# Performance work log

Hardware: AMD Instinct MI355X
Metric: run time of the kernel (lower is better)

The kernel has to match this reference:

```python
import jax, jax.numpy as jnp
import numpy as np

# ---- config (mirrors init_kwargs) ----
H = 128
W = 128
FMO_STEPS = 4
INPUT_FRAMES = 1
N_PIECES = 1
N_TERMS = 2
CAM_DIST = 2.0
ROT_DIVIDE = 1.0
SIGMAINV = 7000.0
ERODE_K = 5
FOCAL = float(1.0 / np.tan(1.57 / 4.0))  # generate_perspective_projection(1.57/2), aspect=1


def quaternion_to_angle_axis(q):
    # q: [B,4] in (w,x,y,z) convention (torchgeometry)
    q1, q2, q3 = q[..., 1], q[..., 2], q[..., 3]
    sin_sq = q1 * q1 + q2 * q2 + q3 * q3
    sin_t = jnp.sqrt(sin_sq + 1e-20)
    cos_t = q[..., 0]
    two_theta = 2.0 * jnp.where(cos_t < 0.0, jnp.arctan2(-sin_t, -cos_t), jnp.arctan2(sin_t, cos_t))
    k = jnp.where(sin_sq > 1e-12, two_theta / sin_t, 2.0)
    return q[..., 1:4] * k[..., None]


def angle_axis_to_rotation_matrix(aa):
    # aa: [B,3] -> [B,3,3] (Rodrigues)
    th = jnp.sqrt(jnp.sum(aa * aa, axis=-1, keepdims=True) + 1e-12)  # [B,1]
    k = aa / th
    kx, ky, kz = k[..., 0], k[..., 1], k[..., 2]
    zero = jnp.zeros_like(kx)
    K = jnp.stack([jnp.stack([zero, -kz, ky], -1),
                   jnp.stack([kz, zero, -kx], -1),
                   jnp.stack([-ky, kx, zero], -1)], -2)
    s = jnp.sin(th)[..., None]
    c = jnp.cos(th)[..., None]
    return jnp.eye(3, dtype=aa.dtype) + s * K + (1.0 - c) * jnp.matmul(K, K)


def rasterize(fv_img, fv_z, face_feat, fn_z):
    # fv_img [B,F,3,2] NDC, fv_z [B,F,3] camera z, face_feat [B,F,3,C], fn_z [B,F]
    B, F = fv_img.shape[:2]
    xs = jnp.linspace(-1.0, 1.0, W)
    ys = jnp.linspace(1.0, -1.0, H)
    py, px = jnp.meshgrid(ys, xs, indexing='ij')  # [H,W]
    a, b, c = fv_img[:, :, 0], fv_img[:, :, 1], fv_img[:, :, 2]  # [B,F,2]
    e0 = b - a
    e1 = c - a
    denom = e0[..., 0] * e1[..., 1] - e0[..., 1] * e1[..., 0]  # [B,F]
    valid = (fn_z > 0.0) & (jnp.abs(denom) > 1e-10)
    inv_den = jnp.where(jnp.abs(denom) > 1e-10, 1.0 / denom, 0.0)
    dx = px[None, None] - a[..., 0][..., None, None]  # [B,F,H,W]
    dy = py[None, None] - a[..., 1][..., None, None]
    w1 = (dx * e1[..., 1][..., None, None] - dy * e1[..., 0][..., None, None]) * inv_den[..., None, None]
    w2 = (e0[..., 0][..., None, None] * dy - e0[..., 1][..., None, None] * dx) * inv_den[..., None, None]
    w0 = 1.0 - w1 - w2
    inside = (w0 >= 0.0) & (w1 >= 0.0) & (w2 >= 0.0) & valid[..., None, None]
    zi = (w0 * fv_z[:, :, 0, None, None] + w1 * fv_z[:, :, 1, None, None] + w2 * fv_z[:, :, 2, None, None])
    score = jnp.where(inside, zi, -1e10)  # camera looks down -z: nearest face has max z
    best = jnp.argmax(score, axis=1)      # [B,H,W] z-buffer winner
    hit = jnp.any(inside, axis=1)
    bary = jnp.stack([w0, w1, w2], axis=-1)  # [B,F,H,W,3]
    idx = jnp.broadcast_to(best[:, None, :, :, None], (B, 1, H, W, 3))
    bary_b = jnp.take_along_axis(bary, idx, axis=1)[:, 0]  # [B,H,W,3]
    feat_b = jax.vmap(lambda f, i: f[i])(face_feat, best)  # [B,H,W,3,C]
    feats = jnp.einsum('bhwkc,bhwk->bhwc', feat_b, bary_b) * hit[..., None]
    # DIB-R soft silhouette: A = 1 - prod(1 - exp(-sigmainv*d^2)), d = dist to triangle, 0 inside
    d2 = None
    tri = (a, b, c)
    for i in range(3):
        p, q = tri[i], tri[(i + 1) % 3]
        ex = (q - p)[..., 0][..., None, None]
        ey = (q - p)[..., 1][..., None, None]
        rx = px[None, None] - p[..., 0][..., None, None]
        ry = py[None, None] - p[..., 1][..., None, None]
        L2 = ex * ex + ey * ey + 1e-12
        t = jnp.clip((rx * ex + ry * ey) / L2, 0.0, 1.0)
        dxe = rx - t * ex
        dye = ry - t * ey
        dd = dxe * dxe + dye * dye
        d2 = dd if d2 is None else jnp.minimum(d2, dd)
    d2 = jnp.where(inside, 0.0, d2)
    prob = jnp.where(valid[..., None, None], jnp.exp(-SIGMAINV * d2), 0.0)
    mask = 1.0 - jnp.prod(1.0 - prob, axis=1)  # [B,H,W]
    return feats, mask


def texture_sample(tex, uv):
    # tex [B,3,Th,Tw], uv [B,H,W,2] in [0,1]; bilinear, v axis flipped (image row 0 <-> v=1)
    Th, Tw = tex.shape[2], tex.shape[3]
    u = jnp.clip(uv[..., 0], 0.0, 1.0) * (Tw - 1)
    v = (1.0 - jnp.clip(uv[..., 1], 0.0, 1.0)) * (Th - 1)
    x0 = jnp.floor(u)
    y0 = jnp.floor(v)
    fx = (u - x0)[:, None]  # [B,1,H,W]
    fy = (v - y0)[:, None]
    x0i = jnp.clip(x0.astype(jnp.int32), 0, Tw - 1)
    x1i = jnp.clip(x0i + 1, 0, Tw - 1)
    y0i = jnp.clip(y0.astype(jnp.int32), 0, Th - 1)
    y1i = jnp.clip(y0i + 1, 0, Th - 1)
    g = jax.vmap(lambda t, yy, xx: t[:, yy, xx])  # [B,3,H,W]
    t00 = g(tex, y0i, x0i)
    t01 = g(tex, y0i, x1i)
    t10 = g(tex, y1i, x0i)
    t11 = g(tex, y1i, x1i)
    return t00 * (1 - fx) * (1 - fy) + t01 * fx * (1 - fy) + t10 * (1 - fx) * fy + t11 * fx * fy


def erode(m, k):
    # kornia erosion with an all-ones kxk kernel == min-pool (geodesic border)
    return -jax.lax.reduce_window(-m, -jnp.inf, jax.lax.max, (1, k, k), (1, 1, 1), 'SAME')


def render_frame(verts_world, faces, face_features, texture_maps):
    # camera at (0,0,CAM_DIST) looking at origin with up=(0,1,0): R_cam == I
    v_cam = verts_world - jnp.array([0.0, 0.0, CAM_DIST], dtype=verts_world.dtype)
    fv_cam = v_cam[:, faces]  # [B,F,3,3]
    n = jnp.cross(fv_cam[:, :, 1] - fv_cam[:, :, 0], fv_cam[:, :, 2] - fv_cam[:, :, 0])
    n = n / (jnp.linalg.norm(n, axis=-1, keepdims=True) + 1e-10)
    fn_z = n[..., 2]
    z = fv_cam[..., 2]  # negative in front of camera
    img = FOCAL * fv_cam[..., :2] / (-z[..., None] + 1e-10)  # [B,F,3,2]
    uv, mask = rasterize(img, z, face_features, fn_z)
    rgb = texture_sample(texture_maps, uv)  # [B,3,H,W]
    mask_e = erode(mask, ERODE_K)
    return jnp.concatenate([rgb, mask_e[:, None]], axis=1)  # [B,4,H,W]


def reference(vertices, translation, quaternion, exp, face_features, texture_maps, faces):
    rot = angle_axis_to_rotation_matrix(quaternion_to_angle_axis(quaternion[:, 0, 0]))
    trans_start = translation[:, :, 0, 0]  # [B,1,3]
    all_renders = []
    renders = []
    frames = 0
    time_before = 0.0
    for pind in range(N_PIECES):
        angles = quaternion_to_angle_axis(quaternion[:, pind, 1]) / ROT_DIVIDE
        rot_step = angle_axis_to_rotation_matrix(exp * angles / FMO_STEPS)
        rot_noexp = angle_axis_to_rotation_matrix(angles * (1.0 - exp))
        n_steps = FMO_STEPS * INPUT_FRAMES // N_PIECES  # prop[pind] (forced for single piece)
        for ti in np.linspace(0.0, 1.0, n_steps):
            if frames == 0:
                time_before = ti
            time_exp = time_before + (ti - time_before) * exp  # [1]
            verts = jnp.einsum('bij,bvj->bvi', rot, vertices) + trans_start
            for p in range(1, N_TERMS):
                verts = verts + (time_exp ** p) * translation[:, :, pind, p]
            renders.append(render_frame(verts, faces, face_features, texture_maps))
            frames += 1
            if frames == FMO_STEPS:
                frames = 0
                all_renders.append(jnp.stack(renders, 1))
                renders = []
                rot = jnp.matmul(rot, rot_noexp)
            else:
                rot = jnp.matmul(rot, rot_step)
        for p in range(1, N_TERMS):
            trans_start = trans_start + translation[:, :, pind, p]
    return jnp.stack(all_renders, 1)  # [B, input_frames, fmo_steps, 4, H, W]


def setup_inputs() -> dict:
    key = jax.random.key(0)
    ks = jax.random.split(key, 7)
    B, V, F = 1, 162, 320
    vertices = jax.random.normal(ks[0], (B, V, 3), jnp.float32) * 0.3
    translation = jax.random.normal(ks[1], (B, 1, N_PIECES, N_TERMS, 3), jnp.float32) * 0.1
    quaternion = jax.random.normal(ks[2], (B, N_PIECES, 2, 4), jnp.float32)
    exp = jax.random.uniform(ks[3], (1,), jnp.float32)
    face_features = jax.random.uniform(ks[4], (B, F, 3, 2), jnp.float32)
    texture_maps = jax.random.uniform(ks[5], (B, 3, 256, 256), jnp.float32)
    faces = jax.random.randint(ks[6], (F, 3), 0, V)
    return {"vertices": vertices, "translation": translation, "quaternion": quaternion,
            "exp": exp, "face_features": face_features, "texture_maps": texture_maps,
            "faces": faces}
```

## Files before the change

kernel.cpp:

```cpp
#include <hip/hip_runtime.h>
#include <math.h>

#define N_FRAMES 4
#define N_FACES  320
#define N_VERTS  162
#define IMG_H    128
#define IMG_W    128
#define FD_STRIDE 20
#define CHUNKS   8



__device__ __forceinline__ void q_to_aa(const float* q, float* aa) {
    float q1 = q[1], q2 = q[2], q3 = q[3];
    float sin_sq = (q1 * q1 + q2 * q2) + q3 * q3;
    float sin_t = sqrtf(sin_sq + 1e-20f);
    float cos_t = q[0];
    float two_theta = (cos_t < 0.0f) ? (2.0f * atan2f(-sin_t, -cos_t))
                                     : (2.0f * atan2f(sin_t, cos_t));
    float k = (sin_sq > 1e-12f) ? (two_theta / sin_t) : 2.0f;
    aa[0] = q1 * k; aa[1] = q2 * k; aa[2] = q3 * k;
}

__device__ __forceinline__ void aa_to_R(const float* aa, float* R) {
    float th = sqrtf(((aa[0] * aa[0] + aa[1] * aa[1]) + aa[2] * aa[2]) + 1e-12f);
    float kx = aa[0] / th, ky = aa[1] / th, kz = aa[2] / th;
    float K[9] = { 0.0f, -kz,  ky,
                   kz,  0.0f, -kx,
                  -ky,   kx, 0.0f };
    float s = sinf(th), c = cosf(th);
    float KK[9];
    for (int i = 0; i < 3; ++i)
        for (int j = 0; j < 3; ++j)
            KK[i*3+j] = (K[i*3+0] * K[0*3+j] + K[i*3+1] * K[1*3+j]) + K[i*3+2] * K[2*3+j];
    float omc = 1.0f - c;
    for (int i = 0; i < 9; ++i) {
        float eye = (i == 0 || i == 4 || i == 8) ? 1.0f : 0.0f;
        R[i] = (eye + s * K[i]) + omc * KK[i];
    }
}

__device__ __forceinline__ void mat3mul(const float* A, const float* B, float* C) {
    for (int i = 0; i < 3; ++i)
        for (int j = 0; j < 3; ++j)
            C[i*3+j] = (A[i*3+0] * B[0*3+j] + A[i*3+1] * B[1*3+j]) + A[i*3+2] * B[2*3+j];
}


__global__ void __launch_bounds__(256)
setup_kernel(const float* __restrict__ verts_in,
             const float* __restrict__ transl,
             const float* __restrict__ quat,
             const float* __restrict__ expv,
             const int*   __restrict__ faces,
             int*   __restrict__ faceCount,
             float* __restrict__ faceData)
{
    __shared__ float rots[N_FRAMES][9];
    __shared__ float sv[N_FRAMES][N_VERTS * 3];
    int tid = threadIdx.x;

    if (tid == 0) {
        float aa0[3], aa1[3], R0[9], step[9];
        q_to_aa(quat, aa0);
        aa_to_R(aa0, R0);
        q_to_aa(quat + 4, aa1);
        float e = expv[0];
        float arg[3];
        for (int i = 0; i < 3; ++i) arg[i] = (e * aa1[i]) / 4.0f;
        aa_to_R(arg, step);
        float cur[9];
        for (int i = 0; i < 9; ++i) { cur[i] = R0[i]; rots[0][i] = R0[i]; }
        for (int k = 1; k < N_FRAMES; ++k) {
            float nxt[9];
            mat3mul(cur, step, nxt);
            for (int i = 0; i < 9; ++i) { cur[i] = nxt[i]; rots[k][i] = nxt[i]; }
        }
    }
    __syncthreads();

    float e = expv[0];
    float t0 = transl[0], t1 = transl[1], t2 = transl[2];
    float u0 = transl[3], u1 = transl[4], u2 = transl[5];

    for (int item = tid; item < N_FRAMES * N_VERTS; item += blockDim.x) {
        int k = item / N_VERTS, v = item - k * N_VERTS;
        float te = (float)((double)k / 3.0) * e;
        float vx = verts_in[v*3+0], vy = verts_in[v*3+1], vz = verts_in[v*3+2];
        const float* R = rots[k];
        float dx_ = (R[0] * vx + R[1] * vy) + R[2] * vz;
        float dy_ = (R[3] * vx + R[4] * vy) + R[5] * vz;
        float dz_ = (R[6] * vx + R[7] * vy) + R[8] * vz;
        float x = (dx_ + t0) + te * u0;
        float y = (dy_ + t1) + te * u1;
        float z = (dz_ + t2) + te * u2;
        z = z - 2.0f;
        sv[k][v*3+0] = x; sv[k][v*3+1] = y; sv[k][v*3+2] = z;
    }
    __syncthreads();

    const float FOCAL = (float)(1.0 / tan(1.57 / 4.0));

    int w    = tid >> 6;
    int lane = tid & 63;
    unsigned long long lmask = (lane == 63) ? 0x7fffffffffffffffull
                                            : ((1ull << lane) - 1ull);
    int cnt = 0;
    for (int base = 0; base < N_FACES; base += 64) {
        int f = base + lane;
        int i0 = faces[f*3+0], i1 = faces[f*3+1], i2 = faces[f*3+2];
        const float* A = &sv[w][i0*3];
        const float* B = &sv[w][i1*3];
        const float* C = &sv[w][i2*3];
        float ux = B[0] - A[0], uy = B[1] - A[1];
        float wx = C[0] - A[0], wy = C[1] - A[1];
        float nz = ux * wy - uy * wx;
        float da = -A[2] + 1e-10f, db = -B[2] + 1e-10f, dc = -C[2] + 1e-10f;
        float ax = (FOCAL * A[0]) / da, ay = (FOCAL * A[1]) / da;
        float bx = (FOCAL * B[0]) / db, by = (FOCAL * B[1]) / db;
        float cx = (FOCAL * C[0]) / dc, cy = (FOCAL * C[1]) / dc;
        float e0x = bx - ax, e0y = by - ay;
        float e1x = cx - ax, e1y = cy - ay;
        float e12x = cx - bx, e12y = cy - by;
        float den = e0x * e1y - e0y * e1x;
        bool dok = fabsf(den) > 1e-10f;
        bool valid = dok && (nz > 0.0f);
        unsigned long long m = __ballot(valid);
        if (valid) {
            float invden = 1.0f / den;
            float L2_0 = (e0x * e0x + e0y * e0y) + 1e-12f;
            float L2_1 = (e12x * e12x + e12y * e12y) + 1e-12f;
            float L2_2 = (e1x * e1x + e1y * e1y) + 1e-12f;
            int pos = cnt + __popcll(m & lmask);
            float4* fd = (float4*)(faceData + (w * N_FACES + pos) * FD_STRIDE);
            fd[0] = make_float4(ax, ay, e0x, e0y);
            fd[1] = make_float4(e1x, e1y, invden, (float)f);
            fd[2] = make_float4(A[2], B[2], C[2], 1.0f / L2_0);
            fd[3] = make_float4(bx, by, e12x, e12y);
            fd[4] = make_float4(cx, cy, 1.0f / L2_1, 1.0f / L2_2);
        }
        cnt += __popcll(m);
    }
    if (lane == 0) faceCount[w] = cnt;
}


__global__ void __launch_bounds__(256)
raster_kernel(const int*   __restrict__ faceCount,
              const float* __restrict__ faceData,
              const float* __restrict__ ffeat,
              const float* __restrict__ tex,
              float* __restrict__ out,
              float* __restrict__ maskbuf)
{
    int frame = blockIdx.x >> 9;
    int blk   = blockIdx.x & 511;
    int tid   = threadIdx.x;
    int chunk = tid & 7;
    int pix   = blk * 32 + (tid >> 3);
    int i = pix >> 7, j = pix & 127;

    int nv = faceCount[frame];

    __shared__ float4 fd4[N_FACES * 5];
    const float4* g = (const float4*)(faceData + frame * N_FACES * FD_STRIDE);
    for (int idx = tid; idx < nv * 5; idx += 256)
        fd4[idx] = g[idx];
    __syncthreads();

    float px = (float)(-1.0 + 2.0 * (double)j / 127.0);
    float py = (float)( 1.0 - 2.0 * (double)i / 127.0);

    float best = -1e10f;
    int bestf = 0;
    float bw0 = 0.0f, bw1 = 0.0f, bw2 = 0.0f;
    float P = 1.0f;

    for (int f = chunk; f < nv; f += CHUNKS) {
        const float4* d = &fd4[f * 5];
        float4 q0 = d[0], q1 = d[1], q2 = d[2], q3 = d[3], q4 = d[4];

        float dx = px - q0.x, dy = py - q0.y;
        float w1 = (dx * q1.y - dy * q1.x) * q1.z;
        float w2 = (q0.z * dy - q0.w * dx) * q1.z;
        float w0 = (1.0f - w1) - w2;
        bool inside = (w0 >= 0.0f) & (w1 >= 0.0f) & (w2 >= 0.0f);
        float zi = (w0 * q2.x + w1 * q2.y) + w2 * q2.z;
        float score = inside ? zi : -1e10f;
        if (score > best) {
            best = score; bestf = (int)q1.w; bw0 = w0; bw1 = w1; bw2 = w2;
        }

        float t0 = fminf(fmaxf((dx * q0.z + dy * q0.w) * q2.w, 0.0f), 1.0f);
        float x0 = dx - t0 * q0.z, y0 = dy - t0 * q0.w;
        float dd = x0 * x0 + y0 * y0;
        float rx1 = px - q3.x, ry1 = py - q3.y;
        float t1 = fminf(fmaxf((rx1 * q3.z + ry1 * q3.w) * q4.z, 0.0f), 1.0f);
        float x1 = rx1 - t1 * q3.z, y1 = ry1 - t1 * q3.w;
        dd = fminf(dd, x1 * x1 + y1 * y1);
        float ex2 = -q1.x, ey2 = -q1.y;
        float rx2 = px - q4.x, ry2 = py - q4.y;
        float t2 = fminf(fmaxf((rx2 * ex2 + ry2 * ey2) * q4.w, 0.0f), 1.0f);
        float x2 = rx2 - t2 * ex2, y2 = ry2 - t2 * ey2;
        dd = fminf(dd, x2 * x2 + y2 * y2);

        float d2 = inside ? 0.0f : dd;
        float prob = __expf(-7000.0f * d2);
        P *= (1.0f - prob);
    }

    for (int m = 1; m <= 4; m <<= 1) {
        float oS = __shfl_xor(best, m);
        int   oF = __shfl_xor(bestf, m);
        float o0 = __shfl_xor(bw0, m);
        float o1 = __shfl_xor(bw1, m);
        float o2 = __shfl_xor(bw2, m);
        bool take = (oS > best) || ((oS == best) && (oF < bestf));
        if (take) { best = oS; bestf = oF; bw0 = o0; bw1 = o1; bw2 = o2; }
        P *= __shfl_xor(P, m);
    }

    if (chunk == 0) {
        bool hit = best != -1e10f;
        float uv0 = 0.0f, uv1 = 0.0f;
        if (hit) {
            const float* fp = ffeat + bestf * 6;
            uv0 = (fp[0] * bw0 + fp[2] * bw1) + fp[4] * bw2;
            uv1 = (fp[1] * bw0 + fp[3] * bw1) + fp[5] * bw2;
        }
        float u = fminf(fmaxf(uv0, 0.0f), 1.0f) * 255.0f;
        float v = (1.0f - fminf(fmaxf(uv1, 0.0f), 1.0f)) * 255.0f;
        float x0f = floorf(u), y0f = floorf(v);
        float fx = u - x0f, fy = v - y0f;
        int x0i = min(max((int)x0f, 0), 255);
        int x1i = min(x0i + 1, 255);
        int y0i = min(max((int)y0f, 0), 255);
        int y1i = min(y0i + 1, 255);

        for (int c = 0; c < 3; ++c) {
            const float* tc = tex + c * 65536;
            float t00 = tc[y0i * 256 + x0i];
            float t01 = tc[y0i * 256 + x1i];
            float t10 = tc[y1i * 256 + x0i];
            float t11 = tc[y1i * 256 + x1i];
            float val = (t00 * (1.0f - fx)) * (1.0f - fy);
            val = val + (t01 * fx) * (1.0f - fy);
            val = val + (t10 * (1.0f - fx)) * fy;
            val = val + (t11 * fx) * fy;
            out[((frame * 4 + c) * IMG_H + i) * IMG_W + j] = val;
        }
        maskbuf[(frame * IMG_H + i) * IMG_W + j] = 1.0f - P;
    }
}


__global__ void __launch_bounds__(256)
erode_kernel(const float* __restrict__ maskbuf, float* __restrict__ out)
{
    int frame = blockIdx.x >> 6;
    int pix = (blockIdx.x & 63) * 256 + threadIdx.x;
    int i = pix >> 7, j = pix & 127;
    float m = 1e30f;
    for (int di = -2; di <= 2; ++di) {
        int ii = i + di;
        if (ii < 0 || ii >= IMG_H) continue;
        for (int dj = -2; dj <= 2; ++dj) {
            int jj = j + dj;
            if (jj < 0 || jj >= IMG_W) continue;
            m = fminf(m, maskbuf[(frame * IMG_H + ii) * IMG_W + jj]);
        }
    }
    out[((frame * 4 + 3) * IMG_H + i) * IMG_W + j] = m;
}


extern "C" void kernel_launch(void* const* d_in, const int* in_sizes, int n_in,
                              void* d_out, int out_size, void* d_ws, size_t ws_size,
                              hipStream_t stream) {
    const float* vertices      = (const float*)d_in[0];
    const float* translation   = (const float*)d_in[1];
    const float* quaternion    = (const float*)d_in[2];
    const float* expv          = (const float*)d_in[3];
    const float* face_features = (const float*)d_in[4];
    const float* texture_maps  = (const float*)d_in[5];
    const int*   faces         = (const int*)d_in[6];
    float* out = (float*)d_out;

    int*   faceCount = (int*)d_ws;
    float* faceData  = (float*)d_ws + 4;
    float* maskbuf   = faceData + N_FRAMES * N_FACES * FD_STRIDE;

    setup_kernel<<<1, 256, 0, stream>>>(vertices, translation, quaternion, expv,
                                        faces, faceCount, faceData);
    raster_kernel<<<N_FRAMES * 512, 256, 0, stream>>>(faceCount, faceData,
                                                      face_features, texture_maps,
                                                      out, maskbuf);
    erode_kernel<<<N_FRAMES * 64, 256, 0, stream>>>(maskbuf, out);
}
```

Before: 96.03 us.

## Cull faces per wave with bounding boxes and split faces across waves

Adds a per-face screen-space bounding box in setup. The raster kernel now gives each wave a 16x4 pixel tile and a strided subset of faces. A wave skips a face with a uniform branch when no pixel in its tile lies within about 0.055 NDC of that box. Partial results are merged across the 8 waves through shared memory instead of lane shuffles, and face data is read from global memory/cache instead of being staged in LDS. The cull threshold drops the soft-silhouette term for distant faces, where exp(-7000*d2) is already near zero, so mask values change very slightly.

```diff
diff --git a/kernel.cpp b/kernel.cpp
--- a/kernel.cpp
+++ b/kernel.cpp
@@ -6,8 +6,8 @@
 #define N_VERTS  162
 #define IMG_H    128
 #define IMG_W    128
-#define FD_STRIDE 20
-#define CHUNKS   8
+#define FD_STRIDE 24
+#define NWAVES   8
 
 
 
@@ -138,6 +138,8 @@
             fd[2] = make_float4(A[2], B[2], C[2], 1.0f / L2_0);
             fd[3] = make_float4(bx, by, e12x, e12y);
             fd[4] = make_float4(cx, cy, 1.0f / L2_1, 1.0f / L2_2);
+            fd[5] = make_float4(fminf(fminf(ax, bx), cx), fminf(fminf(ay, by), cy),
+                                fmaxf(fmaxf(ax, bx), cx), fmaxf(fmaxf(ay, by), cy));
         }
         cnt += __popcll(m);
     }
@@ -145,7 +147,7 @@
 }
 
 
-__global__ void __launch_bounds__(256)
+__global__ void __launch_bounds__(512)
 raster_kernel(const int*   __restrict__ faceCount,
               const float* __restrict__ faceData,
               const float* __restrict__ ffeat,
@@ -153,20 +155,16 @@
               float* __restrict__ out,
               float* __restrict__ maskbuf)
 {
-    int frame = blockIdx.x >> 9;
-    int blk   = blockIdx.x & 511;
+    int frame = blockIdx.x >> 8;
+    int blk   = blockIdx.x & 255;
     int tid   = threadIdx.x;
-    int chunk = tid & 7;
-    int pix   = blk * 32 + (tid >> 3);
-    int i = pix >> 7, j = pix & 127;
+    int lane  = tid & 63;
+    int wv    = __builtin_amdgcn_readfirstlane(tid >> 6);
+    int tile_x = blk & 7, tile_y = blk >> 3;
+    int j = tile_x * 16 + (lane & 15);
+    int i = tile_y * 4 + (lane >> 4);
 
     int nv = faceCount[frame];
-
-    __shared__ float4 fd4[N_FACES * 5];
-    const float4* g = (const float4*)(faceData + frame * N_FACES * FD_STRIDE);
-    for (int idx = tid; idx < nv * 5; idx += 256)
-        fd4[idx] = g[idx];
-    __syncthreads();
 
     float px = (float)(-1.0 + 2.0 * (double)j / 127.0);
     float py = (float)( 1.0 - 2.0 * (double)i / 127.0);
@@ -176,31 +174,43 @@
     float bw0 = 0.0f, bw1 = 0.0f, bw2 = 0.0f;
     float P = 1.0f;
 
-    for (int f = chunk; f < nv; f += CHUNKS) {
-        const float4* d = &fd4[f * 5];
-        float4 q0 = d[0], q1 = d[1], q2 = d[2], q3 = d[3], q4 = d[4];
-
-        float dx = px - q0.x, dy = py - q0.y;
-        float w1 = (dx * q1.y - dy * q1.x) * q1.z;
-        float w2 = (q0.z * dy - q0.w * dx) * q1.z;
+    const float* g = faceData + frame * N_FACES * FD_STRIDE;
+
+    for (int f = wv; f < nv; f += NWAVES) {
+        const float* d = g + f * FD_STRIDE;
+        float xmin = d[20], ymin = d[21], xmax = d[22], ymax = d[23];
+        float cdx = fmaxf(fmaxf(xmin - px, px - xmax), 0.0f);
+        float cdy = fmaxf(fmaxf(ymin - py, py - ymax), 0.0f);
+        bool near = (cdx * cdx + cdy * cdy) <= 0.003f;
+        if (!__any(near)) continue;
+
+        float ax = d[0], ay = d[1], e0x = d[2], e0y = d[3];
+        float e1x = d[4], e1y = d[5], invden = d[6], fidx = d[7];
+        float z0 = d[8], z1 = d[9], z2 = d[10], invL2_0 = d[11];
+        float bx = d[12], by = d[13], e12x = d[14], e12y = d[15];
+        float cx = d[16], cy = d[17], invL2_1 = d[18], invL2_2 = d[19];
+
+        float dx = px - ax, dy = py - ay;
+        float w1 = (dx * e1y - dy * e1x) * invden;
+        float w2 = (e0x * dy - e0y * dx) * invden;
         float w0 = (1.0f - w1) - w2;
         bool inside = (w0 >= 0.0f) & (w1 >= 0.0f) & (w2 >= 0.0f);
-        float zi = (w0 * q2.x + w1 * q2.y) + w2 * q2.z;
+        float zi = (w0 * z0 + w1 * z1) + w2 * z2;
         float score = inside ? zi : -1e10f;
         if (score > best) {
-            best = score; bestf = (int)q1.w; bw0 = w0; bw1 = w1; bw2 = w2;
-        }
-
-        float t0 = fminf(fmaxf((dx * q0.z + dy * q0.w) * q2.w, 0.0f), 1.0f);
-        float x0 = dx - t0 * q0.z, y0 = dy - t0 * q0.w;
+            best = score; bestf = (int)fidx; bw0 = w0; bw1 = w1; bw2 = w2;
+        }
+
+        float t0 = fminf(fmaxf((dx * e0x + dy * e0y) * invL2_0, 0.0f), 1.0f);
+        float x0 = dx - t0 * e0x, y0 = dy - t0 * e0y;
         float dd = x0 * x0 + y0 * y0;
-        float rx1 = px - q3.x, ry1 = py - q3.y;
-        float t1 = fminf(fmaxf((rx1 * q3.z + ry1 * q3.w) * q4.z, 0.0f), 1.0f);
-        float x1 = rx1 - t1 * q3.z, y1 = ry1 - t1 * q3.w;
+        float rx1 = px - bx, ry1 = py - by;
+        float t1 = fminf(fmaxf((rx1 * e12x + ry1 * e12y) * invL2_1, 0.0f), 1.0f);
+        float x1 = rx1 - t1 * e12x, y1 = ry1 - t1 * e12y;
         dd = fminf(dd, x1 * x1 + y1 * y1);
-        float ex2 = -q1.x, ey2 = -q1.y;
-        float rx2 = px - q4.x, ry2 = py - q4.y;
-        float t2 = fminf(fmaxf((rx2 * ex2 + ry2 * ey2) * q4.w, 0.0f), 1.0f);
+        float ex2 = -e1x, ey2 = -e1y;
+        float rx2 = px - cx, ry2 = py - cy;
+        float t2 = fminf(fmaxf((rx2 * ex2 + ry2 * ey2) * invL2_2, 0.0f), 1.0f);
         float x2 = rx2 - t2 * ex2, y2 = ry2 - t2 * ey2;
         dd = fminf(dd, x2 * x2 + y2 * y2);
 
@@ -209,24 +219,32 @@
         P *= (1.0f - prob);
     }
 
-    for (int m = 1; m <= 4; m <<= 1) {
-        float oS = __shfl_xor(best, m);
-        int   oF = __shfl_xor(bestf, m);
-        float o0 = __shfl_xor(bw0, m);
-        float o1 = __shfl_xor(bw1, m);
-        float o2 = __shfl_xor(bw2, m);
-        bool take = (oS > best) || ((oS == best) && (oF < bestf));
-        if (take) { best = oS; bestf = oF; bw0 = o0; bw1 = o1; bw2 = o2; }
-        P *= __shfl_xor(P, m);
-    }
-
-    if (chunk == 0) {
-        bool hit = best != -1e10f;
+    __shared__ float red[512 * 6];
+    float* my = &red[tid * 6];
+    my[0] = best; my[1] = __int_as_float(bestf);
+    my[2] = bw0;  my[3] = bw1; my[4] = bw2; my[5] = P;
+    __syncthreads();
+
+    if (tid < 64) {
+        float bb = red[tid * 6 + 0];
+        int   bf = __float_as_int(red[tid * 6 + 1]);
+        float r0 = red[tid * 6 + 2], r1 = red[tid * 6 + 3], r2 = red[tid * 6 + 4];
+        float Pt = red[tid * 6 + 5];
+        for (int w = 1; w < NWAVES; ++w) {
+            const float* e = &red[(w * 64 + tid) * 6];
+            float s = e[0]; int ff = __float_as_int(e[1]);
+            if ((s > bb) || ((s == bb) && (ff < bf))) {
+                bb = s; bf = ff; r0 = e[2]; r1 = e[3]; r2 = e[4];
+            }
+            Pt *= e[5];
+        }
+
+        bool hit = bb != -1e10f;
         float uv0 = 0.0f, uv1 = 0.0f;
         if (hit) {
-            const float* fp = ffeat + bestf * 6;
-            uv0 = (fp[0] * bw0 + fp[2] * bw1) + fp[4] * bw2;
-            uv1 = (fp[1] * bw0 + fp[3] * bw1) + fp[5] * bw2;
+            const float* fp = ffeat + bf * 6;
+            uv0 = (fp[0] * r0 + fp[2] * r1) + fp[4] * r2;
+            uv1 = (fp[1] * r0 + fp[3] * r1) + fp[5] * r2;
         }
         float u = fminf(fmaxf(uv0, 0.0f), 1.0f) * 255.0f;
         float v = (1.0f - fminf(fmaxf(uv1, 0.0f), 1.0f)) * 255.0f;
@@ -249,7 +267,7 @@
             val = val + (t11 * fx) * fy;
             out[((frame * 4 + c) * IMG_H + i) * IMG_W + j] = val;
         }
-        maskbuf[(frame * IMG_H + i) * IMG_W + j] = 1.0f - P;
+        maskbuf[(frame * IMG_H + i) * IMG_W + j] = 1.0f - Pt;
     }
 }
 
@@ -292,7 +310,7 @@
 
     setup_kernel<<<1, 256, 0, stream>>>(vertices, translation, quaternion, expv,
                                         faces, faceCount, faceData);
-    raster_kernel<<<N_FRAMES * 512, 256, 0, stream>>>(faceCount, faceData,
+    raster_kernel<<<N_FRAMES * 256, 512, 0, stream>>>(faceCount, faceData,
                                                       face_features, texture_maps,
                                                       out, maskbuf);
     erode_kernel<<<N_FRAMES * 64, 256, 0, stream>>>(maskbuf, out);
```

New measurement: 91.67 us. 4.5% less time.
